# Performance work log

Hardware: AMD Instinct MI355X
Metric: run time of the kernel (lower is better)

## Reference

```python
import jax, jax.numpy as jnp
import numpy as np

B, C, H, W = 16, 128, 64, 64
L, ND = 512, 256
GROUPS = 32
EPS = 1e-6


def setup_inputs() -> dict:
    key = jax.random.key(0)
    ks = jax.random.split(key, 8)
    return {
        "x": jax.random.normal(ks[0], (B, C, H, W), dtype=jnp.float32),
        "nd": jax.random.normal(ks[1], (B, L, ND), dtype=jnp.float32),
        "gn_gamma": jnp.ones((C,), dtype=jnp.float32),
        "gn_beta": jnp.zeros((C,), dtype=jnp.float32),
        "q_w": jax.random.normal(ks[2], (C, C), dtype=jnp.float32) * 0.02,
        "q_b": jax.random.normal(ks[3], (C,), dtype=jnp.float32) * 0.02,
        "nd_w": jax.random.normal(ks[4], (C, ND), dtype=jnp.float32) * 0.02,
        "nd_b": jax.random.normal(ks[5], (C,), dtype=jnp.float32) * 0.02,
        "proj_w": jax.random.normal(ks[6], (C, C), dtype=jnp.float32) * 0.02,
        "proj_b": jax.random.normal(ks[7], (C,), dtype=jnp.float32) * 0.02,
    }


def _group_norm(x, gamma, beta):
    b, c, h, w = x.shape
    xr = x.reshape(b, GROUPS, c // GROUPS, h, w)
    mean = xr.mean(axis=(2, 3, 4), keepdims=True)
    var = xr.var(axis=(2, 3, 4), keepdims=True)
    xn = ((xr - mean) * jax.lax.rsqrt(var + EPS)).reshape(b, c, h, w)
    return xn * gamma[None, :, None, None] + beta[None, :, None, None]


def reference(x, nd, gn_gamma, gn_beta, q_w, q_b, nd_w, nd_b, proj_w, proj_b):
    b, c, h, w = x.shape
    hn = _group_norm(x, gn_gamma, gn_beta)
    # 1x1 conv query -> [b, hw, c]
    q = jnp.einsum('bchw,oc->bhwo', hn, q_w).reshape(b, h * w, c) + q_b
    # silu + linear projection of conditioning; k and v use identical projection/input
    kv = jax.nn.silu(nd) @ nd_w.T + nd_b  # [b, L, c]
    # attention: [b, hw, L]
    logits = jnp.einsum('bnc,blc->bnl', q, kv) * (c ** -0.5)
    attn = jax.nn.softmax(logits, axis=2)
    # weighted sum of v -> [b, c, hw] -> [b, c, h, w]
    out = jnp.einsum('blc,bnl->bcn', kv, attn).reshape(b, c, h, w)
    # 1x1 conv projection
    out = jnp.einsum('bchw,oc->bohw', out, proj_w) + proj_b[None, :, None, None]
    return x + out
```

## Files before the change

### kernel.cpp

```cpp
#include <hip/hip_runtime.h>
#include <math.h>

constexpr int kB = 16, kC = 128, kHW = 4096, kL = 512, kND = 256, kG = 32;
constexpr float kEps = 1e-6f;
constexpr float kScale = 0.08838834764831845f;

typedef short sv8 __attribute__((ext_vector_type(8)));
typedef float f32x16 __attribute__((ext_vector_type(16)));

static __device__ __forceinline__ unsigned short f2bf(float f) {
    unsigned int u = __builtin_bit_cast(unsigned int, f);
    u += 0x7fffu + ((u >> 16) & 1u);
    return (unsigned short)(u >> 16);
}
static __device__ __forceinline__ float bf2f(unsigned short s) {
    unsigned int u = ((unsigned int)s) << 16;
    return __builtin_bit_cast(float, u);
}

__global__ __launch_bounds__(256) void gn_stats_k(const float* __restrict__ x,
                                                  float* __restrict__ stats) {
    int bg = blockIdx.x;
    const float4* p4 = (const float4*)(x + (size_t)bg * 4 * kHW);
    int tid = threadIdx.x;
    float s = 0.f, ss = 0.f;
    for (int i = tid; i < 4096; i += 256) {
        float4 v = p4[i];
        s  += (v.x + v.y) + (v.z + v.w);
        ss += (v.x * v.x + v.y * v.y) + (v.z * v.z + v.w * v.w);
    }
#pragma unroll
    for (int off = 1; off < 64; off <<= 1) {
        s  += __shfl_xor(s, off, 64);
        ss += __shfl_xor(ss, off, 64);
    }
    __shared__ float red[8];
    int wid = tid >> 6;
    if ((tid & 63) == 0) { red[wid] = s; red[wid + 4] = ss; }
    __syncthreads();
    if (tid == 0) {
        float S  = (red[0] + red[1]) + (red[2] + red[3]);
        float SS = (red[4] + red[5]) + (red[6] + red[7]);
        float mean = S * (1.f / 16384.f);
        float var  = SS * (1.f / 16384.f) - mean * mean;
        stats[bg * 2]     = mean;
        stats[bg * 2 + 1] = rsqrtf(var + kEps);
    }
}

__global__ __launch_bounds__(256) void prep_k(const float* __restrict__ w,
                                              unsigned short* __restrict__ wb) {
    int i = (blockIdx.x * 256 + threadIdx.x) * 4;
    float4 v = *(const float4*)(w + i);
    wb[i + 0] = f2bf(v.x); wb[i + 1] = f2bf(v.y);
    wb[i + 2] = f2bf(v.z); wb[i + 3] = f2bf(v.w);
}

__global__ __launch_bounds__(256) void kv_k(const float* __restrict__ nd,
                                            const float* __restrict__ nd_w,
                                            const float* __restrict__ nd_b,
                                            unsigned short* __restrict__ kv_bf,
                                            unsigned short* __restrict__ kvT_bf) {
    __shared__ float s_lds[8][256];
    __shared__ float w_lds[128][68];
    __shared__ float t_lds[8][129];
    int b = blockIdx.y;
    int l0 = blockIdx.x * 8;
    int tid = threadIdx.x;
    const float4* ndp = (const float4*)(nd + ((size_t)b * kL + l0) * kND);
#pragma unroll
    for (int r = 0; r < 2; r++) {
        int idx = tid + r * 256;
        int row = idx >> 6;
        int c4 = idx & 63;
        float4 v = ndp[row * 64 + c4];
        v.x = v.x / (1.f + __expf(-v.x));
        v.y = v.y / (1.f + __expf(-v.y));
        v.z = v.z / (1.f + __expf(-v.z));
        v.w = v.w / (1.f + __expf(-v.w));
        *(float4*)&s_lds[row][c4 * 4] = v;
    }
    float acc[4] = {0.f, 0.f, 0.f, 0.f};
    int lr = tid >> 5;
    int oq = tid & 31;
    for (int d0 = 0; d0 < kND; d0 += 64) {
        __syncthreads();
#pragma unroll
        for (int r = 0; r < 8; r++) {
            int idx = tid + r * 256;
            int row = idx >> 4;
            int c4 = idx & 15;
            float4 v = ((const float4*)(nd_w + (size_t)row * kND + d0))[c4];
            *(float4*)&w_lds[row][c4 * 4] = v;
        }
        __syncthreads();
        for (int dd = 0; dd < 64; dd += 4) {
            float4 sv = *(const float4*)&s_lds[lr][d0 + dd];
#pragma unroll
            for (int j = 0; j < 4; j++) {
                float4 wv = *(const float4*)&w_lds[oq + 32 * j][dd];
                acc[j] += sv.x * wv.x + sv.y * wv.y + sv.z * wv.z + sv.w * wv.w;
            }
        }
    }
#pragma unroll
    for (int j = 0; j < 4; j++) {
        int o = oq + 32 * j;
        float vout = acc[j] + nd_b[o];
        kv_bf[((size_t)b * kL + l0 + lr) * kC + o] = f2bf(vout);
        t_lds[lr][o] = vout;
    }
    __syncthreads();
    {
        int o = tid >> 1, lh = (tid & 1) * 4;
        unsigned long long pk = 0;
#pragma unroll
        for (int i = 0; i < 4; i++)
            pk |= (unsigned long long)f2bf(t_lds[lh + i][o]) << (16 * i);
        *(unsigned long long*)(kvT_bf + ((size_t)b * kC + o) * kL + l0 + lh) = pk;
    }
}

__global__ __launch_bounds__(256) void qproj_k(const float* __restrict__ x,
                                               const float* __restrict__ stats,
                                               const float* __restrict__ gamma,
                                               const float* __restrict__ beta,
                                               const float* __restrict__ q_w,
                                               const float* __restrict__ q_b,
                                               unsigned short* __restrict__ q_bf) {
    __shared__ __align__(16) unsigned short smem[17408];
    __shared__ float gab[256];
    const int b = blockIdx.y;
    const int n0 = blockIdx.x * 128;
    const int tid = threadIdx.x;
    const int wave = tid >> 6, lane = tid & 63;
    const int lrow = lane & 31, hi = lane >> 5;

    if (tid < 128) {
        float mean = stats[(b * kG + (tid >> 2)) * 2];
        float rstd = stats[(b * kG + (tid >> 2)) * 2 + 1];
        float ga = gamma[tid] * rstd;
        gab[tid] = ga;
        gab[128 + tid] = beta[tid] - mean * ga;
    }
#pragma unroll
    for (int r = 0; r < 16; r++) {
        int idx = tid + r * 256;
        int row = idx >> 5, c4 = idx & 31;
        float4 v = ((const float4*)q_w)[idx];
        unsigned int lo = (unsigned int)f2bf(v.x) | ((unsigned int)f2bf(v.y) << 16);
        unsigned int h2 = (unsigned int)f2bf(v.z) | ((unsigned int)f2bf(v.w) << 16);
        *(uint2*)&smem[row * 136 + c4 * 4] = make_uint2(lo, h2);
    }
    __syncthreads();

    sv8 qa[8];
    {
        const float* xp = x + (size_t)b * kC * kHW + n0 + wave * 32 + lrow;
#pragma unroll
        for (int kc = 0; kc < 8; kc++) {
            int cb = kc * 16 + hi * 8;
            float4 g0 = *(const float4*)&gab[cb];
            float4 g1 = *(const float4*)&gab[cb + 4];
            float4 e0 = *(const float4*)&gab[128 + cb];
            float4 e1 = *(const float4*)&gab[128 + cb + 4];
            sv8 a;
            a[0] = (short)f2bf(xp[(size_t)(cb + 0) * kHW] * g0.x + e0.x);
            a[1] = (short)f2bf(xp[(size_t)(cb + 1) * kHW] * g0.y + e0.y);
            a[2] = (short)f2bf(xp[(size_t)(cb + 2) * kHW] * g0.z + e0.z);
            a[3] = (short)f2bf(xp[(size_t)(cb + 3) * kHW] * g0.w + e0.w);
            a[4] = (short)f2bf(xp[(size_t)(cb + 4) * kHW] * g1.x + e1.x);
            a[5] = (short)f2bf(xp[(size_t)(cb + 5) * kHW] * g1.y + e1.y);
            a[6] = (short)f2bf(xp[(size_t)(cb + 6) * kHW] * g1.z + e1.z);
            a[7] = (short)f2bf(xp[(size_t)(cb + 7) * kHW] * g1.w + e1.w);
            qa[kc] = a;
        }
    }

    f32x16 dacc[4];
#pragma unroll
    for (int ot = 0; ot < 4; ot++)
#pragma unroll
        for (int r = 0; r < 16; r++) dacc[ot][r] = 0.f;
#pragma unroll
    for (int ot = 0; ot < 4; ot++) {
        const unsigned short* brow = smem + (ot * 32 + lrow) * 136 + hi * 8;
#pragma unroll
        for (int kc = 0; kc < 8; kc++)
            dacc[ot] = __builtin_amdgcn_mfma_f32_32x32x16_bf16(
                           qa[kc], *(const sv8*)(brow + kc * 16), dacc[ot], 0, 0, 0);
    }
    __syncthreads();

#pragma unroll
    for (int ot = 0; ot < 4; ot++) {
        int o = ot * 32 + lrow;
        float qb = q_b[o];
#pragma unroll
        for (int r = 0; r < 16; r++) {
            int n_loc = wave * 32 + (r & 3) + 8 * (r >> 2) + 4 * hi;
            smem[n_loc * 136 + o] = f2bf((dacc[ot][r] + qb) * kScale);
        }
    }
    __syncthreads();
#pragma unroll
    for (int r = 0; r < 8; r++) {
        int idx = tid + r * 256;
        int n = idx >> 4, ch = idx & 15;
        *(uint4*)(q_bf + ((size_t)b * kHW + n0 + n) * kC + ch * 8) =
            *(const uint4*)&smem[n * 136 + ch * 8];
    }
}

__global__ __launch_bounds__(256, 2) void attn_k(
    const unsigned short* __restrict__ qb,
    const unsigned short* __restrict__ kvb,
    const unsigned short* __restrict__ kvtb,
    const unsigned short* __restrict__ pwb,
    const float* __restrict__ proj_b,
    const float* __restrict__ x,
    float* __restrict__ out)
{
    __shared__ __align__(16) unsigned short smem[27136];
    unsigned short* kv_lds  = smem;
    unsigned short* kvt_lds = smem + 8704;
    unsigned short* p_lds   = smem + 17920;
    unsigned short* o_lds   = smem;

    const int b = blockIdx.y;
    const int n0 = blockIdx.x * 128;
    const int tid = threadIdx.x;
    const int wave = tid >> 6;
    const int lane = tid & 63;
    const int lrow = lane & 31;
    const int hi = lane >> 5;

    sv8 qa[8];
    {
        const unsigned short* qrow =
            qb + ((size_t)b * kHW + n0 + wave * 32 + lrow) * kC + hi * 8;
#pragma unroll
        for (int kc = 0; kc < 8; kc++)
            qa[kc] = *(const sv8*)(qrow + kc * 16);
    }

    f32x16 oacc[4];
#pragma unroll
    for (int ct = 0; ct < 4; ct++)
#pragma unroll
        for (int r = 0; r < 16; r++) oacc[ct][r] = 0.f;
    float rsum[16];
#pragma unroll
    for (int r = 0; r < 16; r++) rsum[r] = 0.f;

    unsigned short* myp = p_lds + wave * 2304;

    for (int l0 = 0; l0 < kL; l0 += 64) {
        __syncthreads();
        {
            const uint4* g = (const uint4*)(kvb + ((size_t)b * kL + l0) * kC);
#pragma unroll
            for (int r = 0; r < 4; r++) {
                int idx = tid + r * 256;
                int row = idx >> 4, c8 = idx & 15;
                *(uint4*)(kv_lds + row * 136 + c8 * 8) = g[idx];
            }
            const uint4* gt = (const uint4*)(kvtb + (size_t)b * kC * kL + l0);
#pragma unroll
            for (int r = 0; r < 4; r++) {
                int idx = tid + r * 256;
                int row = idx >> 3, c8 = idx & 7;
                *(uint4*)(kvt_lds + row * 72 + c8 * 8) = gt[row * 64 + c8];
            }
        }
        __syncthreads();

#pragma unroll
        for (int ls = 0; ls < 2; ls++) {
            f32x16 s;
#pragma unroll
            for (int r = 0; r < 16; r++) s[r] = 0.f;
            const unsigned short* brow = kv_lds + (ls * 32 + lrow) * 136 + hi * 8;
#pragma unroll
            for (int kc = 0; kc < 8; kc++)
                s = __builtin_amdgcn_mfma_f32_32x32x16_bf16(
                        qa[kc], *(const sv8*)(brow + kc * 16), s, 0, 0, 0);
#pragma unroll
            for (int r = 0; r < 16; r++) {
                float p = __expf(s[r]);
                rsum[r] += p;
                int n = (r & 3) + 8 * (r >> 2) + 4 * hi;
                myp[n * 72 + ls * 32 + lrow] = f2bf(p);
            }
        }
        sv8 pa[4];
#pragma unroll
        for (int kk = 0; kk < 4; kk++)
            pa[kk] = *(const sv8*)(myp + lrow * 72 + kk * 16 + hi * 8);
#pragma unroll
        for (int ct = 0; ct < 4; ct++) {
            const unsigned short* brow = kvt_lds + (ct * 32 + lrow) * 72 + hi * 8;
#pragma unroll
            for (int kk = 0; kk < 4; kk++)
                oacc[ct] = __builtin_amdgcn_mfma_f32_32x32x16_bf16(
                               pa[kk], *(const sv8*)(brow + kk * 16), oacc[ct], 0, 0, 0);
        }
    }

#pragma unroll
    for (int r = 0; r < 16; r++) {
        float v = rsum[r];
        v += __shfl_xor(v, 1, 64);
        v += __shfl_xor(v, 2, 64);
        v += __shfl_xor(v, 4, 64);
        v += __shfl_xor(v, 8, 64);
        v += __shfl_xor(v, 16, 64);
        rsum[r] = 1.f / v;
    }

    __syncthreads();
#pragma unroll
    for (int ct = 0; ct < 4; ct++)
#pragma unroll
        for (int r = 0; r < 16; r++) {
            int n = wave * 32 + (r & 3) + 8 * (r >> 2) + 4 * hi;
            o_lds[n * 136 + ct * 32 + lrow] = f2bf(oacc[ct][r] * rsum[r]);
        }
    sv8 oa[8];
    {
        const unsigned short* orow = o_lds + (wave * 32 + lrow) * 136 + hi * 8;
#pragma unroll
        for (int kc = 0; kc < 8; kc++) oa[kc] = *(const sv8*)(orow + kc * 16);
    }
    f32x16 dacc[4];
#pragma unroll
    for (int ot = 0; ot < 4; ot++)
#pragma unroll
        for (int r = 0; r < 16; r++) dacc[ot][r] = 0.f;
#pragma unroll
    for (int ot = 0; ot < 4; ot++) {
        const unsigned short* brow = pwb + (ot * 32 + lrow) * kC + hi * 8;
#pragma unroll
        for (int kc = 0; kc < 8; kc++)
            dacc[ot] = __builtin_amdgcn_mfma_f32_32x32x16_bf16(
                           oa[kc], *(const sv8*)(brow + kc * 16), dacc[ot], 0, 0, 0);
    }
#pragma unroll
    for (int ot = 0; ot < 4; ot++)
#pragma unroll
        for (int r = 0; r < 16; r++) {
            int n = wave * 32 + (r & 3) + 8 * (r >> 2) + 4 * hi;
            o_lds[n * 136 + ot * 32 + lrow] = f2bf(dacc[ot][r]);
        }
    __syncthreads();
#pragma unroll 4
    for (int it = 0; it < 64; it++) {
        int idx = it * 256 + tid;
        int o = idx >> 7, n = idx & 127;
        size_t gi = ((size_t)b * kC + o) * kHW + n0 + n;
        out[gi] = bf2f(o_lds[n * 136 + o]) + proj_b[o] + x[gi];
    }
}

extern "C" void kernel_launch(void* const* d_in, const int* in_sizes, int n_in,
                              void* d_out, int out_size, void* d_ws, size_t ws_size,
                              hipStream_t stream) {
    const float* x      = (const float*)d_in[0];
    const float* nd     = (const float*)d_in[1];
    const float* gamma  = (const float*)d_in[2];
    const float* beta   = (const float*)d_in[3];
    const float* q_w    = (const float*)d_in[4];
    const float* q_b    = (const float*)d_in[5];
    const float* nd_w   = (const float*)d_in[6];
    const float* nd_b   = (const float*)d_in[7];
    const float* proj_w = (const float*)d_in[8];
    const float* proj_b = (const float*)d_in[9];
    float* out = (float*)d_out;

    float* stats          = (float*)d_ws;
    unsigned short* pwb   = (unsigned short*)(stats + 1024);
    unsigned short* kv_bf = pwb + 16384;
    unsigned short* kvT_bf = kv_bf + (size_t)kB * kL * kC;
    unsigned short* q_bf  = kvT_bf + (size_t)kB * kL * kC;

    gn_stats_k<<<dim3(kB * kG), dim3(256), 0, stream>>>(x, stats);
    prep_k<<<dim3(16), dim3(256), 0, stream>>>(proj_w, pwb);
    kv_k<<<dim3(kL / 8, kB), dim3(256), 0, stream>>>(nd, nd_w, nd_b, kv_bf, kvT_bf);
    qproj_k<<<dim3(kHW / 128, kB), dim3(256), 0, stream>>>(x, stats, gamma, beta, q_w, q_b, q_bf);
    attn_k<<<dim3(kHW / 128, kB), dim3(256), 0, stream>>>(q_bf, kv_bf, kvT_bf, pwb,
                                                          proj_b, x, out);
}
```

Measured before the change: 99.98 us.

## Prefetch KV tiles into registers, XOR-swizzle LDS, raise attention occupancy

Each step now loads the next KV and KV-transpose tile into registers while the current tile's MFMAs run, and writes them to LDS after a barrier. This hides global load latency behind compute. LDS layouts switch from padded rows to XOR-swizzled rows, which shrinks shared memory so launch bounds can ask for 3 blocks per CU. s_setprio is raised around the MFMA sections. The in-flight prefetch registers plus the higher occupancy target may cause register pressure or spills.

```diff
diff --git a/kernel.cpp b/kernel.cpp
--- a/kernel.cpp
+++ b/kernel.cpp
@@ -212,7 +212,7 @@
     }
 }
 
-__global__ __launch_bounds__(256, 2) void attn_k(
+__global__ __launch_bounds__(256, 3) void attn_k(
     const unsigned short* __restrict__ qb,
     const unsigned short* __restrict__ kvb,
     const unsigned short* __restrict__ kvtb,
@@ -221,11 +221,8 @@
     const float* __restrict__ x,
     float* __restrict__ out)
 {
-    __shared__ __align__(16) unsigned short smem[27136];
-    unsigned short* kv_lds  = smem;
-    unsigned short* kvt_lds = smem + 8704;
-    unsigned short* p_lds   = smem + 17920;
-    unsigned short* o_lds   = smem;
+    __shared__ __align__(16) unsigned short smem[24576];
+    char* base = (char*)smem;
 
     const int b = blockIdx.y;
     const int n0 = blockIdx.x * 128;
@@ -234,6 +231,7 @@
     const int lane = tid & 63;
     const int lrow = lane & 31;
     const int hi = lane >> 5;
+    const int swz_l = (lrow & 7) << 4;
 
     sv8 qa[8];
     {
@@ -253,58 +251,85 @@
 #pragma unroll
     for (int r = 0; r < 16; r++) rsum[r] = 0.f;
 
-    unsigned short* myp = p_lds + wave * 2304;
-
-    for (int l0 = 0; l0 < kL; l0 += 64) {
+    char* pbase = base + 32768 + wave * 4096;
+
+    uint4 pf[8];
+    const uint4* gkv  = (const uint4*)(kvb  + (size_t)b * kL * kC);
+    const uint4* gkvt = (const uint4*)(kvtb + (size_t)b * kC * kL);
+
+    auto issue = [&](int l0) {
+        const uint4* g = gkv + (size_t)l0 * (kC / 8);
+#pragma unroll
+        for (int r = 0; r < 4; r++) pf[r] = g[tid + r * 256];
+        const uint4* gt = gkvt + (l0 >> 3);
+#pragma unroll
+        for (int r = 0; r < 4; r++) {
+            int idx = tid + r * 256;
+            pf[4 + r] = gt[(idx >> 3) * (kL / 8) + (idx & 7)];
+        }
+    };
+    auto commit = [&]() {
+#pragma unroll
+        for (int r = 0; r < 4; r++) {
+            int idx = tid + r * 256;
+            int row = idx >> 4, ch = idx & 15;
+            *(uint4*)(base + ((row * 256 + ch * 16) ^ ((row & 7) << 4))) = pf[r];
+        }
+#pragma unroll
+        for (int r = 0; r < 4; r++) {
+            int idx = tid + r * 256;
+            int row = idx >> 3, ch = idx & 7;
+            *(uint4*)(base + 16384 + ((row * 128 + ch * 16) ^ ((row & 7) << 4))) = pf[4 + r];
+        }
+    };
+
+    issue(0);
+    commit();
+
+    for (int t = 0; t < 8; t++) {
         __syncthreads();
-        {
-            const uint4* g = (const uint4*)(kvb + ((size_t)b * kL + l0) * kC);
-#pragma unroll
-            for (int r = 0; r < 4; r++) {
-                int idx = tid + r * 256;
-                int row = idx >> 4, c8 = idx & 15;
-                *(uint4*)(kv_lds + row * 136 + c8 * 8) = g[idx];
-            }
-            const uint4* gt = (const uint4*)(kvtb + (size_t)b * kC * kL + l0);
-#pragma unroll
-            for (int r = 0; r < 4; r++) {
-                int idx = tid + r * 256;
-                int row = idx >> 3, c8 = idx & 7;
-                *(uint4*)(kvt_lds + row * 72 + c8 * 8) = gt[row * 64 + c8];
-            }
-        }
-        __syncthreads();
+        if (t < 7) issue((t + 1) << 6);
 
 #pragma unroll
         for (int ls = 0; ls < 2; ls++) {
             f32x16 s;
 #pragma unroll
             for (int r = 0; r < 16; r++) s[r] = 0.f;
-            const unsigned short* brow = kv_lds + (ls * 32 + lrow) * 136 + hi * 8;
+            const char* rowp = base + (ls * 32 + lrow) * 256;
+            __builtin_amdgcn_s_setprio(1);
 #pragma unroll
             for (int kc = 0; kc < 8; kc++)
                 s = __builtin_amdgcn_mfma_f32_32x32x16_bf16(
-                        qa[kc], *(const sv8*)(brow + kc * 16), s, 0, 0, 0);
+                        qa[kc], *(const sv8*)(rowp + ((kc * 32 + hi * 16) ^ swz_l)),
+                        s, 0, 0, 0);
+            __builtin_amdgcn_s_setprio(0);
 #pragma unroll
             for (int r = 0; r < 16; r++) {
                 float p = __expf(s[r]);
                 rsum[r] += p;
                 int n = (r & 3) + 8 * (r >> 2) + 4 * hi;
-                myp[n * 72 + ls * 32 + lrow] = f2bf(p);
+                *(unsigned short*)(pbase + n * 128 +
+                    (((ls * 32 + lrow) * 2) ^ ((n & 7) << 4))) = f2bf(p);
             }
         }
         sv8 pa[4];
 #pragma unroll
         for (int kk = 0; kk < 4; kk++)
-            pa[kk] = *(const sv8*)(myp + lrow * 72 + kk * 16 + hi * 8);
+            pa[kk] = *(const sv8*)(pbase + lrow * 128 + ((kk * 32 + hi * 16) ^ swz_l));
+        __builtin_amdgcn_s_setprio(1);
 #pragma unroll
         for (int ct = 0; ct < 4; ct++) {
-            const unsigned short* brow = kvt_lds + (ct * 32 + lrow) * 72 + hi * 8;
+            const char* rowp = base + 16384 + (ct * 32 + lrow) * 128;
 #pragma unroll
             for (int kk = 0; kk < 4; kk++)
                 oacc[ct] = __builtin_amdgcn_mfma_f32_32x32x16_bf16(
-                               pa[kk], *(const sv8*)(brow + kk * 16), oacc[ct], 0, 0, 0);
-        }
+                               pa[kk], *(const sv8*)(rowp + ((kk * 32 + hi * 16) ^ swz_l)),
+                               oacc[ct], 0, 0, 0);
+        }
+        __builtin_amdgcn_s_setprio(0);
+
+        __syncthreads();
+        if (t < 7) commit();
     }
 
 #pragma unroll
@@ -318,6 +343,7 @@
         rsum[r] = 1.f / v;
     }
 
+    unsigned short* o_lds = smem;
     __syncthreads();
 #pragma unroll
     for (int ct = 0; ct < 4; ct++)
```

After: 210.0 us. 2.1x slower.

## Read K/V MFMA operands directly from global memory instead of LDS staging

Applied to the files above, without the earlier changes.

Drops the per-tile cooperative copy of kv and kv-transpose into shared memory, along with the two block barriers around it. Each wave now loads its MFMA B operands straight from global memory (relying on L1/L2 caching), and the LDS allocation shrinks to just the P scratch and the output tile. It also wraps the MFMA loops in s_setprio and removes the 2-blocks-per-SM launch bound. The trade is more redundant global/L1 traffic and exposed load latency per wave in exchange for no barriers and less LDS, which may allow higher occupancy.

```diff
diff --git a/kernel.cpp b/kernel.cpp
--- a/kernel.cpp
+++ b/kernel.cpp
@@ -212,7 +212,7 @@
     }
 }
 
-__global__ __launch_bounds__(256, 2) void attn_k(
+__global__ __launch_bounds__(256) void attn_k(
     const unsigned short* __restrict__ qb,
     const unsigned short* __restrict__ kvb,
     const unsigned short* __restrict__ kvtb,
@@ -221,11 +221,7 @@
     const float* __restrict__ x,
     float* __restrict__ out)
 {
-    __shared__ __align__(16) unsigned short smem[27136];
-    unsigned short* kv_lds  = smem;
-    unsigned short* kvt_lds = smem + 8704;
-    unsigned short* p_lds   = smem + 17920;
-    unsigned short* o_lds   = smem;
+    __shared__ __align__(16) unsigned short smem[17408];
 
     const int b = blockIdx.y;
     const int n0 = blockIdx.x * 128;
@@ -253,38 +249,23 @@
 #pragma unroll
     for (int r = 0; r < 16; r++) rsum[r] = 0.f;
 
-    unsigned short* myp = p_lds + wave * 2304;
+    unsigned short* myp = smem + wave * 2304;
+    const unsigned short* kvB  = kvb  + (size_t)b * kL * kC;
+    const unsigned short* kvtB = kvtb + (size_t)b * kC * kL;
 
     for (int l0 = 0; l0 < kL; l0 += 64) {
-        __syncthreads();
-        {
-            const uint4* g = (const uint4*)(kvb + ((size_t)b * kL + l0) * kC);
-#pragma unroll
-            for (int r = 0; r < 4; r++) {
-                int idx = tid + r * 256;
-                int row = idx >> 4, c8 = idx & 15;
-                *(uint4*)(kv_lds + row * 136 + c8 * 8) = g[idx];
-            }
-            const uint4* gt = (const uint4*)(kvtb + (size_t)b * kC * kL + l0);
-#pragma unroll
-            for (int r = 0; r < 4; r++) {
-                int idx = tid + r * 256;
-                int row = idx >> 3, c8 = idx & 7;
-                *(uint4*)(kvt_lds + row * 72 + c8 * 8) = gt[row * 64 + c8];
-            }
-        }
-        __syncthreads();
-
 #pragma unroll
         for (int ls = 0; ls < 2; ls++) {
             f32x16 s;
 #pragma unroll
             for (int r = 0; r < 16; r++) s[r] = 0.f;
-            const unsigned short* brow = kv_lds + (ls * 32 + lrow) * 136 + hi * 8;
+            const unsigned short* brow = kvB + (size_t)(l0 + ls * 32 + lrow) * kC + hi * 8;
+            __builtin_amdgcn_s_setprio(1);
 #pragma unroll
             for (int kc = 0; kc < 8; kc++)
                 s = __builtin_amdgcn_mfma_f32_32x32x16_bf16(
                         qa[kc], *(const sv8*)(brow + kc * 16), s, 0, 0, 0);
+            __builtin_amdgcn_s_setprio(0);
 #pragma unroll
             for (int r = 0; r < 16; r++) {
                 float p = __expf(s[r]);
@@ -297,14 +278,16 @@
 #pragma unroll
         for (int kk = 0; kk < 4; kk++)
             pa[kk] = *(const sv8*)(myp + lrow * 72 + kk * 16 + hi * 8);
+        __builtin_amdgcn_s_setprio(1);
 #pragma unroll
         for (int ct = 0; ct < 4; ct++) {
-            const unsigned short* brow = kvt_lds + (ct * 32 + lrow) * 72 + hi * 8;
+            const unsigned short* brow = kvtB + (size_t)(ct * 32 + lrow) * kL + l0 + hi * 8;
 #pragma unroll
             for (int kk = 0; kk < 4; kk++)
                 oacc[ct] = __builtin_amdgcn_mfma_f32_32x32x16_bf16(
                                pa[kk], *(const sv8*)(brow + kk * 16), oacc[ct], 0, 0, 0);
         }
+        __builtin_amdgcn_s_setprio(0);
     }
 
 #pragma unroll
@@ -318,6 +301,7 @@
         rsum[r] = 1.f / v;
     }
 
+    unsigned short* o_lds = smem;
     __syncthreads();
 #pragma unroll
     for (int ct = 0; ct < 4; ct++)
```

Result: slower. 138.5 us (+38.5%).
